# Performance work log

Measured on AMD Instinct MI355X. Metric: run time of the kernel, lower is better.

Reference implementation:

```python
import jax, jax.numpy as jnp
import numpy as np

EPS = 1e-15
MAX_ATANH = 1.0 - 1e-5
V = 2097152   # total nodes (B*N*L flattened)
E = 8388608   # edges, ~avg degree 4 (temporal + parent/child)
ATT = 16
MAXD = 512    # mixer embedding table size
# curvature c = 1.0 (registered buffer, constant)


def _mobius_add(a, b):
    # Poincare ball Mobius addition, c = 1
    a2 = jnp.sum(a * a, -1, keepdims=True)
    b2 = jnp.sum(b * b, -1, keepdims=True)
    ab = jnp.sum(a * b, -1, keepdims=True)
    num = (1.0 + 2.0 * ab + b2) * a + (1.0 - a2) * b
    den = 1.0 + 2.0 * ab + a2 * b2
    return num / jnp.maximum(den, EPS)


def _log_map_x(x, y):
    # log_x(y): tangent vector at x pointing to y (c = 1)
    sub = _mobius_add(-x, y)
    n = jnp.maximum(jnp.linalg.norm(sub, axis=-1, keepdims=True), EPS)
    lam = 2.0 / jnp.maximum(1.0 - jnp.sum(x * x, -1, keepdims=True), EPS)
    return (2.0 / lam) * jnp.arctanh(jnp.minimum(n, MAX_ATANH)) * (sub / n)


def _exp_map_x(x, v):
    # exp_x(v) (c = 1)
    n = jnp.maximum(jnp.linalg.norm(v, axis=-1, keepdims=True), EPS)
    lam = 2.0 / jnp.maximum(1.0 - jnp.sum(x * x, -1, keepdims=True), EPS)
    return _mobius_add(x, jnp.tanh(0.5 * lam * n) * (v / n))


def setup_inputs() -> dict:
    key = jax.random.key(0)
    ks = jax.random.split(key, 8)
    # node embeddings strictly inside the unit ball: exp0 of a small tangent vec
    v0 = 0.5 * jax.random.normal(ks[0], (V, 2), jnp.float32)
    n0 = jnp.maximum(jnp.linalg.norm(v0, axis=-1, keepdims=True), EPS)
    x = jnp.tanh(n0) * v0 / n0
    edge_index = jax.random.randint(ks[1], (2, E), 0, V)
    depth = jax.random.randint(ks[2], (V,), 0, MAXD)
    W1 = jax.random.normal(ks[3], (2, ATT), jnp.float32) / jnp.sqrt(2.0)
    b1 = 0.1 * jax.random.normal(ks[4], (ATT,), jnp.float32)
    W2 = jax.random.normal(ks[5], (ATT, 1), jnp.float32) / jnp.sqrt(float(ATT))
    eta = jnp.float32(1.0)
    depth_scale = 1.0 + 0.01 * jax.random.normal(ks[6], (MAXD,), jnp.float32)
    depth_theta = 0.01 * jax.random.normal(ks[7], (MAXD,), jnp.float32)
    return {"x": x, "W1": W1, "b1": b1, "W2": W2, "eta": eta,
            "depth_scale": depth_scale, "depth_theta": depth_theta,
            "edge_index": edge_index, "depth": depth}


def reference(x, W1, b1, W2, eta, depth_scale, depth_theta, edge_index, depth):
    row, col = edge_index[0], edge_index[1]
    xi = x[row]                      # [E,2] gather target endpoints
    xj = x[col]                      # [E,2] gather source endpoints
    v_ij = _log_map_x(xi, xj)        # [E,2] hyperbolic log-map
    # small per-edge MLP scorer: Linear(2,16) -> GELU(exact) -> Linear(16,1)
    h = jax.nn.gelu(v_ij @ W1 + b1, approximate=False)
    scores = (h @ W2)[:, 0]          # [E]
    # segment softmax over target node (row)
    mx = jax.ops.segment_max(scores, row, num_segments=V)
    e = jnp.exp(scores - mx[row])
    den = jax.ops.segment_sum(e, row, num_segments=V)
    alpha = e / jnp.maximum(den[row], EPS)
    # scatter-add aggregate in tangent space
    m = jax.ops.segment_sum(alpha[:, None] * v_ij, row, num_segments=V)  # [V,2]
    # depth-gated mixer: per-node scale + 2D rotation
    d = jnp.minimum(depth, MAXD - 1)
    k = depth_scale[d][:, None]
    ang = depth_theta[d]
    ca, sa = jnp.cos(ang), jnp.sin(ang)
    m = k * jnp.stack([ca * m[:, 0] - sa * m[:, 1],
                       sa * m[:, 0] + ca * m[:, 1]], axis=-1)
    # exp-map update
    return _exp_map_x(x, eta * m)
```

## Files before the change

### kernel.cpp

```cpp
#include <hip/hip_runtime.h>
#include <math.h>

#define EPSF 1e-15f
#define MAX_ATANH (1.0f - 1e-5f)
#define ATT 16

#define LOG_NPB 11
#define NPB (1 << LOG_NPB)
#define MAXB 1024
#define NBLK 1024

__device__ __forceinline__ float fast_gelu(float u) {
    const float x  = fabsf(u) * 0.70710678118654752f;
    const float w  = __fdividef(1.0f, fmaf(0.3275911f, x, 1.0f));
    float p = 1.061405429f;
    p = fmaf(p, w, -1.453152027f);
    p = fmaf(p, w,  1.421413741f);
    p = fmaf(p, w, -0.284496736f);
    p = fmaf(p, w,  0.254829592f);
    const float e    = __expf(-0.5f * u * u);
    const float erfp = fmaf(-p * w, e, 1.0f);
    const float er   = copysignf(erfp, u);
    return 0.5f * u * (1.0f + er);
}

__device__ __forceinline__ float fast_atanh(float z) {
    return 0.5f * __logf(__fdividef(1.0f + z, 1.0f - z));
}

__device__ __forceinline__ float fast_tanh(float z) {
    return 1.0f - __fdividef(2.0f, __expf(2.0f * z) + 1.0f);
}

__global__ void __launch_bounds__(256) hist_kernel(const int* __restrict__ row,
                                                   int E, int B,
                                                   unsigned* __restrict__ counts ) {
    __shared__ unsigned h[MAXB];
    for (int i = threadIdx.x; i < B; i += 256) h[i] = 0u;
    __syncthreads();
    const int T = gridDim.x * 256;
    const int nv = E >> 2;
    const int4* row4 = (const int4*)row;
    for (int i = blockIdx.x * 256 + threadIdx.x; i < nv; i += T) {
        const int4 r = row4[i];
        atomicAdd(&h[((unsigned)r.x) >> LOG_NPB], 1u);
        atomicAdd(&h[((unsigned)r.y) >> LOG_NPB], 1u);
        atomicAdd(&h[((unsigned)r.z) >> LOG_NPB], 1u);
        atomicAdd(&h[((unsigned)r.w) >> LOG_NPB], 1u);
    }
    for (int e = (nv << 2) + blockIdx.x * 256 + threadIdx.x; e < E; e += T)
        atomicAdd(&h[((unsigned)row[e]) >> LOG_NPB], 1u);
    __syncthreads();
    for (int i = threadIdx.x; i < B; i += 256)
        counts[(size_t)i * gridDim.x + blockIdx.x] = h[i];
}

__global__ void __launch_bounds__(256) scan_blocks_kernel(const unsigned* __restrict__ counts,
                                                          unsigned* __restrict__ within,
                                                          unsigned* __restrict__ totals) {
    const int b = blockIdx.x;
    const unsigned* src = counts + (size_t)b * NBLK;
    unsigned* dst = within + (size_t)b * NBLK;
    __shared__ unsigned s[256];
    unsigned v0, v1, v2, v3;
    {
        const uint4 v = ((const uint4*)src)[threadIdx.x];
        v0 = v.x; v1 = v.y; v2 = v.z; v3 = v.w;
    }
    s[threadIdx.x] = v0 + v1 + v2 + v3;
    __syncthreads();
    for (int off = 1; off < 256; off <<= 1) {
        unsigned t = (threadIdx.x >= off) ? s[threadIdx.x - off] : 0u;
        __syncthreads();
        s[threadIdx.x] += t;
        __syncthreads();
    }
    unsigned base = (threadIdx.x > 0) ? s[threadIdx.x - 1] : 0u;
    uint4 o;
    o.x = base; o.y = o.x + v0; o.z = o.y + v1; o.w = o.z + v2;
    ((uint4*)dst)[threadIdx.x] = o;
    if (threadIdx.x == 255) totals[b] = s[255];
}

__global__ void __launch_bounds__(256) scan_totals_kernel(const unsigned* __restrict__ totals,
                                                          unsigned* __restrict__ base, int B) {
    __shared__ unsigned s[256];
    unsigned v0 = 0, v1 = 0, v2 = 0, v3 = 0;
    const int i0 = threadIdx.x * 4;
    if (i0 + 3 < B) {
        const uint4 v = ((const uint4*)totals)[threadIdx.x];
        v0 = v.x; v1 = v.y; v2 = v.z; v3 = v.w;
    } else {
        if (i0 + 0 < B) v0 = totals[i0 + 0];
        if (i0 + 1 < B) v1 = totals[i0 + 1];
        if (i0 + 2 < B) v2 = totals[i0 + 2];
        if (i0 + 3 < B) v3 = totals[i0 + 3];
    }
    s[threadIdx.x] = v0 + v1 + v2 + v3;
    __syncthreads();
    for (int off = 1; off < 256; off <<= 1) {
        unsigned t = (threadIdx.x >= off) ? s[threadIdx.x - off] : 0u;
        __syncthreads();
        s[threadIdx.x] += t;
        __syncthreads();
    }
    unsigned b0 = (threadIdx.x > 0) ? s[threadIdx.x - 1] : 0u;
    if (i0 + 0 < B) base[i0 + 0] = b0;           b0 += v0;
    if (i0 + 1 < B) base[i0 + 1] = b0;           b0 += v1;
    if (i0 + 2 < B) base[i0 + 2] = b0;           b0 += v2;
    if (i0 + 3 < B) base[i0 + 3] = b0;           b0 += v3;
    if (threadIdx.x == 255) base[B] = s[255];
}

__global__ void __launch_bounds__(256) scatter_kernel(const int* __restrict__ row,
                                                      const int* __restrict__ col,
                                                      int E, int B,
                                                      const unsigned* __restrict__ base,
                                                      const unsigned* __restrict__ within,
                                                      unsigned* __restrict__ payload) {
    __shared__ unsigned cur[MAXB];
    const int nblk = gridDim.x;
    for (int i = threadIdx.x; i < B; i += 256)
        cur[i] = base[i] + within[(size_t)i * nblk + blockIdx.x];
    __syncthreads();
    const int T = nblk * 256;
    const int nv = E >> 2;
    const int4* row4 = (const int4*)row;
    const int4* col4 = (const int4*)col;
    for (int i = blockIdx.x * 256 + threadIdx.x; i < nv; i += T) {
        const int4 r = row4[i];
        const int4 c = col4[i];
        {
            const unsigned rr = (unsigned)r.x;
            const unsigned pos = atomicAdd(&cur[rr >> LOG_NPB], 1u);
            payload[pos] = ((rr & (NPB - 1)) << 21) | (unsigned)c.x;
        }
        {
            const unsigned rr = (unsigned)r.y;
            const unsigned pos = atomicAdd(&cur[rr >> LOG_NPB], 1u);
            payload[pos] = ((rr & (NPB - 1)) << 21) | (unsigned)c.y;
        }
        {
            const unsigned rr = (unsigned)r.z;
            const unsigned pos = atomicAdd(&cur[rr >> LOG_NPB], 1u);
            payload[pos] = ((rr & (NPB - 1)) << 21) | (unsigned)c.z;
        }
        {
            const unsigned rr = (unsigned)r.w;
            const unsigned pos = atomicAdd(&cur[rr >> LOG_NPB], 1u);
            payload[pos] = ((rr & (NPB - 1)) << 21) | (unsigned)c.w;
        }
    }
    for (int e = (nv << 2) + blockIdx.x * 256 + threadIdx.x; e < E; e += T) {
        const unsigned rr = (unsigned)row[e];
        const unsigned pos = atomicAdd(&cur[rr >> LOG_NPB], 1u);
        payload[pos] = ((rr & (NPB - 1)) << 21) | (unsigned)col[e];
    }
}

__global__ void __launch_bounds__(1024) bucket_reduce_kernel(
        const float2* __restrict__ x,
        const float* __restrict__ W1,
        const float* __restrict__ b1,
        const float* __restrict__ W2,
        const unsigned* __restrict__ base,
        const unsigned* __restrict__ payload,
        const int* __restrict__ depth,
        const float* __restrict__ depth_scale,
        const float* __restrict__ depth_theta,
        const float* __restrict__ eta_p,
        float2* __restrict__ out, int V) {
    __shared__ float sden[NPB];
    __shared__ float smx[NPB];
    __shared__ float smy[NPB];
    const int b = blockIdx.x;
    const int nodeBase = b << LOG_NPB;
    for (int i = threadIdx.x; i < NPB; i += blockDim.x) {
        sden[i] = 0.f; smx[i] = 0.f; smy[i] = 0.f;
    }
    __syncthreads();

    const unsigned e0 = base[b], e1 = base[b + 1];
    for (unsigned e = e0 + threadIdx.x; e < e1; e += blockDim.x) {
        const unsigned p = payload[e];
        const unsigned lrow = p >> 21;
        const unsigned c = p & 0x1FFFFFu;
        const float2 xi = x[nodeBase + (int)lrow];
        const float2 xj = x[c];

        const float ax = -xi.x, ay = -xi.y;
        const float bx = xj.x,  by = xj.y;
        const float a2 = ax * ax + ay * ay;
        const float b2 = bx * bx + by * by;
        const float ab = ax * bx + ay * by;
        const float ca = 1.0f + 2.0f * ab + b2;
        const float cb = 1.0f - a2;
        const float dn = fmaxf(1.0f + 2.0f * ab + a2 * b2, EPSF);
        const float rdn = __fdividef(1.0f, dn);
        const float subx = (ca * ax + cb * bx) * rdn;
        const float suby = (ca * ay + cb * by) * rdn;

        const float n = fmaxf(sqrtf(subx * subx + suby * suby), EPSF);
        const float M = fmaxf(1.0f - (xi.x * xi.x + xi.y * xi.y), EPSF);
        const float scl = M * fast_atanh(fminf(n, MAX_ATANH)) * __fdividef(1.0f, n);
        const float vx = scl * subx;
        const float vy = scl * suby;

        float s = 0.0f;
        #pragma unroll
        for (int k = 0; k < ATT; ++k) {
            const float u = fmaf(vx, W1[k], fmaf(vy, W1[ATT + k], b1[k]));
            s = fmaf(fast_gelu(u), W2[k], s);
        }

        const float ee = __expf(s);
        atomicAdd(&sden[lrow], ee);
        atomicAdd(&smx[lrow], ee * vx);
        atomicAdd(&smy[lrow], ee * vy);
    }
    __syncthreads();

    const float eta = eta_p[0];
    for (int i = threadIdx.x; i < NPB; i += blockDim.x) {
        const int v = nodeBase + i;
        if (v >= V) break;
        const float rdv = __fdividef(1.0f, fmaxf(sden[i], EPSF));
        const float mx = smx[i] * rdv;
        const float my = smy[i] * rdv;

        const int d = min(depth[v], 511);
        const float k   = depth_scale[d];
        const float ang = depth_theta[d];
        const float cs = __cosf(ang), sn = __sinf(ang);
        const float m0 = eta * (k * (cs * mx - sn * my));
        const float m1 = eta * (k * (sn * mx + cs * my));

        const float2 xi = x[v];

        const float n = fmaxf(sqrtf(m0 * m0 + m1 * m1), EPSF);
        const float M = fmaxf(1.0f - (xi.x * xi.x + xi.y * xi.y), EPSF);
        const float t = fast_tanh(__fdividef(n, M));
        const float tn = t * __fdividef(1.0f, n);
        const float bx = tn * m0;
        const float by = tn * m1;

        const float a2 = xi.x * xi.x + xi.y * xi.y;
        const float b2 = bx * bx + by * by;
        const float ab = xi.x * bx + xi.y * by;
        const float ca = 1.0f + 2.0f * ab + b2;
        const float cb = 1.0f - a2;
        const float dn = fmaxf(1.0f + 2.0f * ab + a2 * b2, EPSF);
        const float rdn = __fdividef(1.0f, dn);

        out[v] = make_float2((ca * xi.x + cb * bx) * rdn,
                             (ca * xi.y + cb * by) * rdn);
    }
}

extern "C" void kernel_launch(void* const* d_in, const int* in_sizes, int n_in,
                              void* d_out, int out_size, void* d_ws, size_t ws_size,
                              hipStream_t stream) {
    const float2* x          = (const float2*)d_in[0];
    const float*  W1         = (const float*)d_in[1];
    const float*  b1         = (const float*)d_in[2];
    const float*  W2         = (const float*)d_in[3];
    const float*  eta        = (const float*)d_in[4];
    const float*  dscale     = (const float*)d_in[5];
    const float*  dtheta     = (const float*)d_in[6];
    const int*    edge_index = (const int*)d_in[7];
    const int*    depth      = (const int*)d_in[8];

    const int V = in_sizes[0] / 2;
    const int E = in_sizes[7] / 2;
    const int B = (V + NPB - 1) >> LOG_NPB;

    const int* row = edge_index;
    const int* col = edge_index + E;

    unsigned* payload = (unsigned*)d_ws;
    unsigned* counts  = payload + E;
    unsigned* within  = counts + (size_t)B * NBLK;
    unsigned* totals  = within + (size_t)B * NBLK;
    unsigned* base    = totals + B;

    hist_kernel<<<NBLK, 256, 0, stream>>>(row, E, B, counts);
    scan_blocks_kernel<<<B, 256, 0, stream>>>(counts, within, totals);
    scan_totals_kernel<<<1, 256, 0, stream>>>(totals, base, B);
    scatter_kernel<<<NBLK, 256, 0, stream>>>(row, col, E, B, base, within, payload);
    bucket_reduce_kernel<<<B, 1024, 0, stream>>>(x, W1, b1, W2, base, payload,
                                                 depth, dscale, dtheta, eta,
                                                 (float2*)d_out, V);
}
```

Baseline: 285.6 us.

## Halve bucket size, shrink scatter grid, cache bucket node coords in LDS

The bucket size drops from 2048 to 1024 nodes, which doubles the bucket count to 2048, and the histogram/scatter grid drops to 512 blocks. The scan kernels are adapted to the new widths. The reduce kernel now runs 512 threads with launch bounds allowing 8 blocks per CU, and it stages the bucket's own node coordinates in shared memory so each edge reads them from LDS instead of global memory. The aim is more reduce blocks, better occupancy and fewer global gathers, paid for with a larger per-block histogram in shared memory and more scatter targets.

```diff
diff --git a/kernel.cpp b/kernel.cpp
--- a/kernel.cpp
+++ b/kernel.cpp
@@ -5,10 +5,10 @@
 #define MAX_ATANH (1.0f - 1e-5f)
 #define ATT 16
 
-#define LOG_NPB 11
+#define LOG_NPB 10
 #define NPB (1 << LOG_NPB)
-#define MAXB 1024
-#define NBLK 1024
+#define MAXB 2048
+#define NBLK 512
 
 __device__ __forceinline__ float fast_gelu(float u) {
     const float x  = fabsf(u) * 0.70710678118654752f;
@@ -62,12 +62,12 @@
     const unsigned* src = counts + (size_t)b * NBLK;
     unsigned* dst = within + (size_t)b * NBLK;
     __shared__ unsigned s[256];
-    unsigned v0, v1, v2, v3;
+    unsigned v0, v1;
     {
-        const uint4 v = ((const uint4*)src)[threadIdx.x];
-        v0 = v.x; v1 = v.y; v2 = v.z; v3 = v.w;
-    }
-    s[threadIdx.x] = v0 + v1 + v2 + v3;
+        const uint2 v = ((const uint2*)src)[threadIdx.x];
+        v0 = v.x; v1 = v.y;
+    }
+    s[threadIdx.x] = v0 + v1;
     __syncthreads();
     for (int off = 1; off < 256; off <<= 1) {
         unsigned t = (threadIdx.x >= off) ? s[threadIdx.x - off] : 0u;
@@ -76,27 +76,24 @@
         __syncthreads();
     }
     unsigned base = (threadIdx.x > 0) ? s[threadIdx.x - 1] : 0u;
-    uint4 o;
-    o.x = base; o.y = o.x + v0; o.z = o.y + v1; o.w = o.z + v2;
-    ((uint4*)dst)[threadIdx.x] = o;
+    uint2 o;
+    o.x = base; o.y = base + v0;
+    ((uint2*)dst)[threadIdx.x] = o;
     if (threadIdx.x == 255) totals[b] = s[255];
 }
 
 __global__ void __launch_bounds__(256) scan_totals_kernel(const unsigned* __restrict__ totals,
                                                           unsigned* __restrict__ base, int B) {
     __shared__ unsigned s[256];
-    unsigned v0 = 0, v1 = 0, v2 = 0, v3 = 0;
-    const int i0 = threadIdx.x * 4;
-    if (i0 + 3 < B) {
-        const uint4 v = ((const uint4*)totals)[threadIdx.x];
-        v0 = v.x; v1 = v.y; v2 = v.z; v3 = v.w;
-    } else {
-        if (i0 + 0 < B) v0 = totals[i0 + 0];
-        if (i0 + 1 < B) v1 = totals[i0 + 1];
-        if (i0 + 2 < B) v2 = totals[i0 + 2];
-        if (i0 + 3 < B) v3 = totals[i0 + 3];
-    }
-    s[threadIdx.x] = v0 + v1 + v2 + v3;
+    unsigned vals[8];
+    const int i0 = threadIdx.x * 8;
+    unsigned sum = 0u;
+    #pragma unroll
+    for (int k = 0; k < 8; ++k) {
+        vals[k] = (i0 + k < B) ? totals[i0 + k] : 0u;
+        sum += vals[k];
+    }
+    s[threadIdx.x] = sum;
     __syncthreads();
     for (int off = 1; off < 256; off <<= 1) {
         unsigned t = (threadIdx.x >= off) ? s[threadIdx.x - off] : 0u;
@@ -105,10 +102,11 @@
         __syncthreads();
     }
     unsigned b0 = (threadIdx.x > 0) ? s[threadIdx.x - 1] : 0u;
-    if (i0 + 0 < B) base[i0 + 0] = b0;           b0 += v0;
-    if (i0 + 1 < B) base[i0 + 1] = b0;           b0 += v1;
-    if (i0 + 2 < B) base[i0 + 2] = b0;           b0 += v2;
-    if (i0 + 3 < B) base[i0 + 3] = b0;           b0 += v3;
+    #pragma unroll
+    for (int k = 0; k < 8; ++k) {
+        if (i0 + k < B) base[i0 + k] = b0;
+        b0 += vals[k];
+    }
     if (threadIdx.x == 255) base[B] = s[255];
 }
 
@@ -158,7 +156,7 @@
     }
 }
 
-__global__ void __launch_bounds__(1024) bucket_reduce_kernel(
+__global__ void __launch_bounds__(512, 8) bucket_reduce_kernel(
         const float2* __restrict__ x,
         const float* __restrict__ W1,
         const float* __restrict__ b1,
@@ -170,22 +168,24 @@
         const float* __restrict__ depth_theta,
         const float* __restrict__ eta_p,
         float2* __restrict__ out, int V) {
-    __shared__ float sden[NPB];
-    __shared__ float smx[NPB];
-    __shared__ float smy[NPB];
+    __shared__ float  sden[NPB];
+    __shared__ float  smx[NPB];
+    __shared__ float  smy[NPB];
+    __shared__ float2 sxi[NPB];
     const int b = blockIdx.x;
     const int nodeBase = b << LOG_NPB;
-    for (int i = threadIdx.x; i < NPB; i += blockDim.x) {
+    for (int i = threadIdx.x; i < NPB; i += 512) {
         sden[i] = 0.f; smx[i] = 0.f; smy[i] = 0.f;
+        sxi[i] = x[nodeBase + i];
     }
     __syncthreads();
 
     const unsigned e0 = base[b], e1 = base[b + 1];
-    for (unsigned e = e0 + threadIdx.x; e < e1; e += blockDim.x) {
+    for (unsigned e = e0 + threadIdx.x; e < e1; e += 512) {
         const unsigned p = payload[e];
         const unsigned lrow = p >> 21;
         const unsigned c = p & 0x1FFFFFu;
-        const float2 xi = x[nodeBase + (int)lrow];
+        const float2 xi = sxi[lrow];
         const float2 xj = x[c];
 
         const float ax = -xi.x, ay = -xi.y;
@@ -221,7 +221,7 @@
     __syncthreads();
 
     const float eta = eta_p[0];
-    for (int i = threadIdx.x; i < NPB; i += blockDim.x) {
+    for (int i = threadIdx.x; i < NPB; i += 512) {
         const int v = nodeBase + i;
         if (v >= V) break;
         const float rdv = __fdividef(1.0f, fmaxf(sden[i], EPSF));
@@ -235,7 +235,7 @@
         const float m0 = eta * (k * (cs * mx - sn * my));
         const float m1 = eta * (k * (sn * mx + cs * my));
 
-        const float2 xi = x[v];
+        const float2 xi = sxi[i];
 
         const float n = fmaxf(sqrtf(m0 * m0 + m1 * m1), EPSF);
         const float M = fmaxf(1.0f - (xi.x * xi.x + xi.y * xi.y), EPSF);
@@ -287,7 +287,7 @@
     scan_blocks_kernel<<<B, 256, 0, stream>>>(counts, within, totals);
     scan_totals_kernel<<<1, 256, 0, stream>>>(totals, base, B);
     scatter_kernel<<<NBLK, 256, 0, stream>>>(row, col, E, B, base, within, payload);
-    bucket_reduce_kernel<<<B, 1024, 0, stream>>>(x, W1, b1, W2, base, payload,
-                                                 depth, dscale, dtheta, eta,
-                                                 (float2*)d_out, V);
-}
+    bucket_reduce_kernel<<<B, 512, 0, stream>>>(x, W1, b1, W2, base, payload,
+                                                depth, dscale, dtheta, eta,
+                                                (float2*)d_out, V);
+}
```

Measured after the change: 275.4 us. 3.6% less time.
